# Performance work log

Hardware: AMD Instinct MI355X
Metric: run time of the kernel (lower is better)

The kernel has to match this reference:

```python
import jax, jax.numpy as jnp
import numpy as np

B, H = 1024, 1024
HID, RHID = 128, 64
DT = 1.0
EPS = 1e-6
SCALES = np.array([0.01, 0.02, 2000.0, 5.0], dtype=np.float32)  # R0[ohm], R1[ohm], C1[F], Q[Ah]


def analytic_ocv(soc):
    # smooth analytic open-circuit-voltage curve (Li-ion-like)
    return 3.0 + 1.2 * soc - 0.5 * soc * soc + 0.3 * soc * soc * soc


def setup_inputs() -> dict:
    key = jax.random.key(0)
    ks = jax.random.split(key, 12)
    inp = {
        "V": jax.random.normal(ks[0], (B, H), jnp.float32),
        "I": jax.random.normal(ks[1], (B, H), jnp.float32),
        "Tz": jax.random.normal(ks[2], (B, H), jnp.float32),
        "soc0": jax.random.uniform(ks[3], (B,), jnp.float32),
        # ParamHead: (soc, I, T) -> 4 positive ECM params
        "W1p": jax.random.normal(ks[4], (3, HID), jnp.float32) / np.sqrt(3.0),
        "b1p": jnp.zeros((HID,), jnp.float32),
        "W2p": jax.random.normal(ks[5], (HID, 4), jnp.float32) / np.sqrt(HID),
        "b2p": jnp.zeros((4,), jnp.float32),
        # ResidualNN: (soc, I, T) -> scalar voltage correction
        "W1r": jax.random.normal(ks[6], (3, RHID), jnp.float32) / np.sqrt(3.0),
        "b1r": jnp.zeros((RHID,), jnp.float32),
        "W2r": jax.random.normal(ks[7], (RHID, 1), jnp.float32) / np.sqrt(RHID),
        "b2r": jnp.zeros((1,), jnp.float32),
    }
    return inp


def _rollout(I, Tz, soc0, W1p, b1p, W2p, b2p, W1r, b1r, W2r, b2r):
    scales = jnp.asarray(SCALES)

    def step(carry, inp_t):
        soc, v1 = carry                       # (B,), (B,)
        I_t, T_t = inp_t                      # (B,), (B,)
        feats = jnp.stack([soc, I_t, T_t], axis=-1)  # (B,3)
        # ParamHead MLP -> positive params via softplus*scale + eps
        hp = jnp.tanh(feats @ W1p + b1p)
        params = jax.nn.softplus(hp @ W2p + b2p) * scales + EPS  # (B,4)
        R0, R1, C1, Q = params[:, 0], params[:, 1], params[:, 2], params[:, 3]
        # ResidualNN correction
        hr = jnp.tanh(feats @ W1r + b1r)
        resid = (hr @ W2r + b2r)[:, 0]        # (B,)
        # Euler ODE updates: RC polarization branch + coulomb counting
        v1_new = v1 + DT * (-v1 / (R1 * C1) + I_t / C1)
        soc_new = jnp.clip(soc - DT * I_t / (Q * 3600.0), 0.0, 1.0)
        V_pred = analytic_ocv(soc_new) - I_t * R0 - v1_new + resid
        return (soc_new, v1_new), V_pred

    carry0 = (soc0, jnp.zeros_like(soc0))
    xs = (I.T, Tz.T)                          # time-major (H,B)
    _, V_pred = jax.lax.scan(step, carry0, xs)
    return V_pred.T                           # (B,H)


def reference(V, I, Tz, soc0, W1p, b1p, W2p, b2p, W1r, b1r, W2r, b2r):
    soc0 = jnp.where(jnp.isnan(soc0), 0.8, soc0)  # default soc0=0.8 semantics
    return _rollout(I, Tz, soc0, W1p, b1p, W2p, b2p, W1r, b1r, W2r, b2r)
```

## Files before the change

kernel.cpp:

```cpp
#include <hip/hip_runtime.h>


#define NB 1024
#define HT 1024
#define HIDN 128
#define RHIDN 64

typedef unsigned uint2v __attribute__((ext_vector_type(2)));

__device__ __forceinline__ float readlane_f(float v, int lane) {
    int r = __builtin_amdgcn_readlane(__builtin_bit_cast(int, v), lane);
    return __builtin_bit_cast(float, r);
}

template <int CTRL, int RMASK>
__device__ __forceinline__ float dpp_add(float x) {
    int s = __builtin_amdgcn_update_dpp(0, __builtin_bit_cast(int, x),
                                        CTRL, RMASK, 0xF, true);
    return x + __builtin_bit_cast(float, s);
}

__device__ __forceinline__ void permlane32_swap(float& a, float& b) {
    uint2v r = __builtin_amdgcn_permlane32_swap(
        __builtin_bit_cast(unsigned, a), __builtin_bit_cast(unsigned, b),
        false, false);
    a = __builtin_bit_cast(float, r[0]);
    b = __builtin_bit_cast(float, r[1]);
}

__device__ __forceinline__ float swz_xor16(float x) {
    int r = __builtin_amdgcn_ds_swizzle(__builtin_bit_cast(int, x), 0x401F);
    return __builtin_bit_cast(float, r);
}

__device__ __forceinline__ float wave_sum(float x) {
    x = dpp_add<0x111, 0xF>(x);
    x = dpp_add<0x112, 0xF>(x);
    x = dpp_add<0x114, 0xF>(x);
    x = dpp_add<0x118, 0xF>(x);
    x = dpp_add<0x142, 0xA>(x);
    x = dpp_add<0x143, 0xC>(x);
    return readlane_f(x, 63);
}

__device__ __forceinline__ float tanh_fast(float x) {
    float t = __builtin_amdgcn_exp2f(x * 2.88539008177793f);
    float r = __builtin_amdgcn_rcpf(t + 1.0f);
    return fmaf(-2.0f, r, 1.0f);
}

__device__ __forceinline__ float softplus_fast(float x) {
    float e = __builtin_amdgcn_exp2f(x * 1.44269504088896f);
    return 0.693147180559945f * __builtin_amdgcn_logf(e + 1.0f);
}

__global__ __launch_bounds__(64, 1) void rollout_kernel(
    const float* __restrict__ Iin, const float* __restrict__ Tzin,
    const float* __restrict__ soc0,
    const float* __restrict__ W1p, const float* __restrict__ b1p,
    const float* __restrict__ W2p, const float* __restrict__ b2p,
    const float* __restrict__ W1r, const float* __restrict__ b1r,
    const float* __restrict__ W2r, const float* __restrict__ b2r,
    float* __restrict__ out)
{
    const int b    = blockIdx.x;
    const int lane = threadIdx.x;
    const int ja = lane, jb = lane + 64;
    const int row = lane >> 4;
    const bool oddrow = (row & 1) != 0;

    const float scaleLane = (row == 0) ? 0.01f : (row == 1) ? 2000.0f
                          : (row == 2) ? 0.02f : 5.0f;

    const float w1pa0 = W1p[0 * HIDN + ja], w1pa1 = W1p[1 * HIDN + ja], w1pa2 = W1p[2 * HIDN + ja];
    const float w1pb0 = W1p[0 * HIDN + jb], w1pb1 = W1p[1 * HIDN + jb], w1pb2 = W1p[2 * HIDN + jb];
    const float bpa = b1p[ja], bpb = b1p[jb];
    const float w2pa0 = W2p[ja * 4 + 0], w2pa1 = W2p[ja * 4 + 1],
                w2pa2 = W2p[ja * 4 + 2], w2pa3 = W2p[ja * 4 + 3];
    const float w2pb0 = W2p[jb * 4 + 0], w2pb1 = W2p[jb * 4 + 1],
                w2pb2 = W2p[jb * 4 + 2], w2pb3 = W2p[jb * 4 + 3];
    const float w1r0 = W1r[0 * RHIDN + lane], w1r1 = W1r[1 * RHIDN + lane], w1r2 = W1r[2 * RHIDN + lane];
    const float brr  = b1r[lane];
    const float w2rr = W2r[lane];
    const float b2p0 = b2p[0], b2p1 = b2p[1], b2p2 = b2p[2], b2p3 = b2p[3];
    const float b2rr = b2r[0];

    const float biasLane = (row == 0) ? b2p0 : (row == 1) ? b2p2
                         : (row == 2) ? b2p1 : b2p3;

    float socv = soc0[b];
    {   unsigned u = __builtin_bit_cast(unsigned, socv);
        if ((u & 0x7FFFFFFFu) > 0x7F800000u) socv = 0.8f; }
    float v1 = 0.0f;

    const float* Ib = Iin  + (size_t)b * HT;
    const float* Tb = Tzin + (size_t)b * HT;
    float*       Ob = out  + (size_t)b * HT;

    float Inext = Ib[lane];
    float Tnext = Tb[lane];

    for (int t0 = 0; t0 < HT; t0 += 64) {
        const float Ibuf = Inext;
        const float Tbuf = Tnext;
        const int t1 = t0 + 64;
        if (t1 < HT) { Inext = Ib[t1 + lane]; Tnext = Tb[t1 + lane]; }

        float Vbuf = 0.0f;
        #pragma unroll 4
        for (int s = 0; s < 64; ++s) {
            const float It = readlane_f(Ibuf, s);
            const float Tt = readlane_f(Tbuf, s);

            const float za = fmaf(Tt, w1pa2, fmaf(It, w1pa1, fmaf(socv, w1pa0, bpa)));
            const float zb = fmaf(Tt, w1pb2, fmaf(It, w1pb1, fmaf(socv, w1pb0, bpb)));
            const float ha = tanh_fast(za);
            const float hb = tanh_fast(zb);

            float p0 = fmaf(hb, w2pb0, ha * w2pa0);
            float p1 = fmaf(hb, w2pb1, ha * w2pa1);
            float p2 = fmaf(hb, w2pb2, ha * w2pa2);
            float p3 = fmaf(hb, w2pb3, ha * w2pa3);

            const float zr  = fmaf(Tt, w1r2, fmaf(It, w1r1, fmaf(socv, w1r0, brr)));
            const float prr = tanh_fast(zr) * w2rr;

            permlane32_swap(p0, p1); float ab = p0 + p1;
            permlane32_swap(p2, p3); float cd = p2 + p3;
            ab += swz_xor16(ab);
            cd += swz_xor16(cd);
            float z = oddrow ? cd : ab;
            z = dpp_add<0x111, 0xF>(z);
            z = dpp_add<0x112, 0xF>(z);
            z = dpp_add<0x114, 0xF>(z);
            z = dpp_add<0x118, 0xF>(z);

            const float resid = wave_sum(prr) + b2rr;

            const float sp   = softplus_fast(z + biasLane);
            const float par  = fmaf(sp, scaleLane, 1e-6f);
            const float ipar = __builtin_amdgcn_rcpf(par);
            const float R0    = readlane_f(par, 15);
            const float invC1 = readlane_f(ipar, 31);
            const float invR1 = readlane_f(ipar, 47);
            const float invQ  = readlane_f(ipar, 63);

            const float invR1C1 = invR1 * invC1;
            v1 = v1 + fmaf(-v1, invR1C1, It * invC1);

            socv = fmaf(It * invQ, -2.77777777777778e-4f, socv);
            socv = fminf(fmaxf(socv, 0.0f), 1.0f);

            const float ocv = fmaf(socv, fmaf(socv, fmaf(socv, 0.3f, -0.5f), 1.2f), 3.0f);
            const float Vp  = (fmaf(-It, R0, ocv) - v1) + resid;

            Vbuf = (lane == s) ? Vp : Vbuf;
        }
        Ob[t0 + lane] = Vbuf;
    }
}

extern "C" void kernel_launch(void* const* d_in, const int* in_sizes, int n_in,
                              void* d_out, int out_size, void* d_ws, size_t ws_size,
                              hipStream_t stream) {
    const float* Iin  = (const float*)d_in[1];
    const float* Tzin = (const float*)d_in[2];
    const float* soc0 = (const float*)d_in[3];
    const float* W1p  = (const float*)d_in[4];
    const float* b1p  = (const float*)d_in[5];
    const float* W2p  = (const float*)d_in[6];
    const float* b2p  = (const float*)d_in[7];
    const float* W1r  = (const float*)d_in[8];
    const float* b1r  = (const float*)d_in[9];
    const float* W2r  = (const float*)d_in[10];
    const float* b2r  = (const float*)d_in[11];
    float* out = (float*)d_out;

    hipLaunchKernelGGL(rollout_kernel, dim3(NB), dim3(64), 0, stream,
                       Iin, Tzin, soc0, W1p, b1p, W2p, b2p, W1r, b1r, W2r, b2r, out);
}
```

Before: 299.7 us.

## Offload residual MLP and output to second wave, pipelined over chunks

Measured after the change: 276.6 us. 1.08x faster.

```diff
diff --git a/kernel.cpp b/kernel.cpp
--- a/kernel.cpp
+++ b/kernel.cpp
@@ -4,7 +4,11 @@
 #define NB 1024
 #define HT 1024
 #define HIDN 128
-#define RHIDN 64
+#define NCHUNK 16
+
+#define K2  2.885390081777927f
+#define KL  1.4426950408889634f
+#define LN2 0.6931471805599453f
 
 typedef unsigned uint2v __attribute__((ext_vector_type(2)));
 
@@ -33,28 +37,13 @@
     return __builtin_bit_cast(float, r);
 }
 
-__device__ __forceinline__ float wave_sum(float x) {
-    x = dpp_add<0x111, 0xF>(x);
-    x = dpp_add<0x112, 0xF>(x);
-    x = dpp_add<0x114, 0xF>(x);
-    x = dpp_add<0x118, 0xF>(x);
-    x = dpp_add<0x142, 0xA>(x);
-    x = dpp_add<0x143, 0xC>(x);
-    return readlane_f(x, 63);
-}
-
-__device__ __forceinline__ float tanh_fast(float x) {
-    float t = __builtin_amdgcn_exp2f(x * 2.88539008177793f);
+__device__ __forceinline__ float tanh_ps(float z) {
+    float t = __builtin_amdgcn_exp2f(z);
     float r = __builtin_amdgcn_rcpf(t + 1.0f);
     return fmaf(-2.0f, r, 1.0f);
 }
 
-__device__ __forceinline__ float softplus_fast(float x) {
-    float e = __builtin_amdgcn_exp2f(x * 1.44269504088896f);
-    return 0.693147180559945f * __builtin_amdgcn_logf(e + 1.0f);
-}
-
-__global__ __launch_bounds__(64, 1) void rollout_kernel(
+__global__ __launch_bounds__(128, 1) void rollout_kernel(
     const float* __restrict__ Iin, const float* __restrict__ Tzin,
     const float* __restrict__ soc0,
     const float* __restrict__ W1p, const float* __restrict__ b1p,
@@ -64,99 +53,130 @@
     float* __restrict__ out)
 {
     const int b    = blockIdx.x;
-    const int lane = threadIdx.x;
-    const int ja = lane, jb = lane + 64;
-    const int row = lane >> 4;
-    const bool oddrow = (row & 1) != 0;
-
-    const float scaleLane = (row == 0) ? 0.01f : (row == 1) ? 2000.0f
-                          : (row == 2) ? 0.02f : 5.0f;
-
-    const float w1pa0 = W1p[0 * HIDN + ja], w1pa1 = W1p[1 * HIDN + ja], w1pa2 = W1p[2 * HIDN + ja];
-    const float w1pb0 = W1p[0 * HIDN + jb], w1pb1 = W1p[1 * HIDN + jb], w1pb2 = W1p[2 * HIDN + jb];
-    const float bpa = b1p[ja], bpb = b1p[jb];
-    const float w2pa0 = W2p[ja * 4 + 0], w2pa1 = W2p[ja * 4 + 1],
-                w2pa2 = W2p[ja * 4 + 2], w2pa3 = W2p[ja * 4 + 3];
-    const float w2pb0 = W2p[jb * 4 + 0], w2pb1 = W2p[jb * 4 + 1],
-                w2pb2 = W2p[jb * 4 + 2], w2pb3 = W2p[jb * 4 + 3];
-    const float w1r0 = W1r[0 * RHIDN + lane], w1r1 = W1r[1 * RHIDN + lane], w1r2 = W1r[2 * RHIDN + lane];
-    const float brr  = b1r[lane];
-    const float w2rr = W2r[lane];
-    const float b2p0 = b2p[0], b2p1 = b2p[1], b2p2 = b2p[2], b2p3 = b2p[3];
-    const float b2rr = b2r[0];
-
-    const float biasLane = (row == 0) ? b2p0 : (row == 1) ? b2p2
-                         : (row == 2) ? b2p1 : b2p3;
-
-    float socv = soc0[b];
-    {   unsigned u = __builtin_bit_cast(unsigned, socv);
-        if ((u & 0x7FFFFFFFu) > 0x7F800000u) socv = 0.8f; }
-    float v1 = 0.0f;
+    const int wid  = threadIdx.x >> 6;
+    const int lane = threadIdx.x & 63;
+
+    __shared__ float4 handBuf[2][64];
+    __shared__ float4 coefS[64];
+    __shared__ float  w2rS[64];
 
     const float* Ib = Iin  + (size_t)b * HT;
     const float* Tb = Tzin + (size_t)b * HT;
     float*       Ob = out  + (size_t)b * HT;
-
-    float Inext = Ib[lane];
-    float Tnext = Tb[lane];
-
-    for (int t0 = 0; t0 < HT; t0 += 64) {
-        const float Ibuf = Inext;
-        const float Tbuf = Tnext;
-        const int t1 = t0 + 64;
-        if (t1 < HT) { Inext = Ib[t1 + lane]; Tnext = Tb[t1 + lane]; }
-
-        float Vbuf = 0.0f;
-        #pragma unroll 4
-        for (int s = 0; s < 64; ++s) {
-            const float It = readlane_f(Ibuf, s);
-            const float Tt = readlane_f(Tbuf, s);
-
-            const float za = fmaf(Tt, w1pa2, fmaf(It, w1pa1, fmaf(socv, w1pa0, bpa)));
-            const float zb = fmaf(Tt, w1pb2, fmaf(It, w1pb1, fmaf(socv, w1pb0, bpb)));
-            const float ha = tanh_fast(za);
-            const float hb = tanh_fast(zb);
-
-            float p0 = fmaf(hb, w2pb0, ha * w2pa0);
-            float p1 = fmaf(hb, w2pb1, ha * w2pa1);
-            float p2 = fmaf(hb, w2pb2, ha * w2pa2);
-            float p3 = fmaf(hb, w2pb3, ha * w2pa3);
-
-            const float zr  = fmaf(Tt, w1r2, fmaf(It, w1r1, fmaf(socv, w1r0, brr)));
-            const float prr = tanh_fast(zr) * w2rr;
-
-            permlane32_swap(p0, p1); float ab = p0 + p1;
-            permlane32_swap(p2, p3); float cd = p2 + p3;
-            ab += swz_xor16(ab);
-            cd += swz_xor16(cd);
-            float z = oddrow ? cd : ab;
-            z = dpp_add<0x111, 0xF>(z);
-            z = dpp_add<0x112, 0xF>(z);
-            z = dpp_add<0x114, 0xF>(z);
-            z = dpp_add<0x118, 0xF>(z);
-
-            const float resid = wave_sum(prr) + b2rr;
-
-            const float sp   = softplus_fast(z + biasLane);
-            const float par  = fmaf(sp, scaleLane, 1e-6f);
-            const float ipar = __builtin_amdgcn_rcpf(par);
-            const float R0    = readlane_f(par, 15);
-            const float invC1 = readlane_f(ipar, 31);
-            const float invR1 = readlane_f(ipar, 47);
-            const float invQ  = readlane_f(ipar, 63);
-
-            const float invR1C1 = invR1 * invC1;
-            v1 = v1 + fmaf(-v1, invR1C1, It * invC1);
-
-            socv = fmaf(It * invQ, -2.77777777777778e-4f, socv);
-            socv = fminf(fmaxf(socv, 0.0f), 1.0f);
-
-            const float ocv = fmaf(socv, fmaf(socv, fmaf(socv, 0.3f, -0.5f), 1.2f), 3.0f);
-            const float Vp  = (fmaf(-It, R0, ocv) - v1) + resid;
-
-            Vbuf = (lane == s) ? Vp : Vbuf;
+    const float b2rr = b2r[0];
+
+    float w1pa0=0,w1pa1=0,w1pa2=0,bpa=0, w1pb0=0,w1pb1=0,w1pb2=0,bpb=0;
+    float w2pa0=0,w2pa1=0,w2pa2=0,w2pa3=0, w2pb0=0,w2pb1=0,w2pb2=0,w2pb3=0;
+    float biasLane=0, scaleLane=0;
+    float socv=0, v1=0, Inext=0, Tnext=0;
+    const int row = lane >> 4;
+    const bool oddrow = (row & 1) != 0;
+
+    if (wid == 0) {
+        const int ja = lane, jb = lane + 64;
+        w1pa0 = W1p[0*HIDN+ja]*K2; w1pa1 = W1p[1*HIDN+ja]*K2; w1pa2 = W1p[2*HIDN+ja]*K2;
+        w1pb0 = W1p[0*HIDN+jb]*K2; w1pb1 = W1p[1*HIDN+jb]*K2; w1pb2 = W1p[2*HIDN+jb]*K2;
+        bpa = b1p[ja]*K2; bpb = b1p[jb]*K2;
+        w2pa0 = W2p[ja*4+0]*KL; w2pa1 = W2p[ja*4+1]*KL;
+        w2pa2 = W2p[ja*4+2]*KL; w2pa3 = W2p[ja*4+3]*KL;
+        w2pb0 = W2p[jb*4+0]*KL; w2pb1 = W2p[jb*4+1]*KL;
+        w2pb2 = W2p[jb*4+2]*KL; w2pb3 = W2p[jb*4+3]*KL;
+        const float b2p0 = b2p[0], b2p1 = b2p[1], b2p2 = b2p[2], b2p3 = b2p[3];
+        biasLane  = ((row == 0) ? b2p0 : (row == 1) ? b2p2 : (row == 2) ? b2p1 : b2p3) * KL;
+        scaleLane = ((row == 0) ? 0.01f : (row == 1) ? 2000.0f : (row == 2) ? 0.02f : 5.0f) * LN2;
+
+        socv = soc0[b];
+        unsigned u = __builtin_bit_cast(unsigned, socv);
+        if ((u & 0x7FFFFFFFu) > 0x7F800000u) socv = 0.8f;
+        v1 = 0.0f;
+        Inext = Ib[lane];
+        Tnext = Tb[lane];
+    }
+
+    for (int c = 0; c <= NCHUNK; ++c) {
+        if (wid == 0) {
+            if (c < NCHUNK) {
+                const float Ibuf = Inext;
+                const float Tbuf = Tnext;
+                const int t1 = (c + 1) * 64;
+                if (t1 < HT) { Inext = Ib[t1 + lane]; Tnext = Tb[t1 + lane]; }
+
+                float4 hand = make_float4(0.f, 0.f, 0.f, 0.f);
+                #pragma unroll 4
+                for (int s = 0; s < 64; ++s) {
+                    const float It = readlane_f(Ibuf, s);
+                    const float Tt = readlane_f(Tbuf, s);
+                    const float carry = socv;
+
+                    const float za = fmaf(Tt, w1pa2, fmaf(It, w1pa1, fmaf(socv, w1pa0, bpa)));
+                    const float zb = fmaf(Tt, w1pb2, fmaf(It, w1pb1, fmaf(socv, w1pb0, bpb)));
+                    const float ha = tanh_ps(za);
+                    const float hb = tanh_ps(zb);
+
+                    float p0 = fmaf(hb, w2pb0, ha * w2pa0);
+                    float p1 = fmaf(hb, w2pb1, ha * w2pa1);
+                    float p2 = fmaf(hb, w2pb2, ha * w2pa2);
+                    float p3 = fmaf(hb, w2pb3, ha * w2pa3);
+
+                    permlane32_swap(p0, p1); float ab = p0 + p1;
+                    permlane32_swap(p2, p3); float cd = p2 + p3;
+                    ab += swz_xor16(ab);
+                    cd += swz_xor16(cd);
+                    float z = oddrow ? cd : ab;
+                    z = dpp_add<0x111, 0xF>(z);
+                    z = dpp_add<0x112, 0xF>(z);
+                    z = dpp_add<0x114, 0xF>(z);
+                    z = dpp_add<0x118, 0xF>(z);
+
+                    const float e   = __builtin_amdgcn_exp2f(z + biasLane);
+                    const float lg  = __builtin_amdgcn_logf(e + 1.0f);
+                    const float par = fmaf(lg, scaleLane, 1e-6f);
+                    const float ipar = __builtin_amdgcn_rcpf(par);
+                    const float R0    = readlane_f(par, 15);
+                    const float invC1 = readlane_f(ipar, 31);
+                    const float invR1 = readlane_f(ipar, 47);
+                    const float invQ  = readlane_f(ipar, 63);
+
+                    const float invR1C1 = invR1 * invC1;
+                    v1 = v1 + fmaf(-v1, invR1C1, It * invC1);
+                    socv = fmaf(It * invQ, -2.77777777777778e-4f, socv);
+                    socv = __builtin_amdgcn_fmed3f(socv, 0.0f, 1.0f);
+
+                    const bool m = (lane == s);
+                    hand.x = m ? carry : hand.x;
+                    hand.y = m ? socv  : hand.y;
+                    hand.z = m ? v1    : hand.z;
+                    hand.w = m ? R0    : hand.w;
+                }
+                handBuf[c & 1][lane] = hand;
+            }
+        } else {
+            if (c == 0) {
+                coefS[lane] = make_float4(W1r[0*64+lane]*K2, W1r[1*64+lane]*K2,
+                                          W1r[2*64+lane]*K2, b1r[lane]*K2);
+                w2rS[lane] = W2r[lane];
+            } else {
+                const int cc = c - 1;
+                const float4 h  = handBuf[cc & 1][lane];
+                const float  Is = Ib[cc * 64 + lane];
+                const float  Ts = Tb[cc * 64 + lane];
+
+                float acc = b2rr;
+                #pragma unroll 8
+                for (int j = 0; j < 64; ++j) {
+                    const float4 w  = coefS[j];
+                    const float  wr = w2rS[j];
+                    const float z  = fmaf(Ts, w.z, fmaf(Is, w.y, fmaf(h.x, w.x, w.w)));
+                    acc = fmaf(tanh_ps(z), wr, acc);
+                }
+
+                const float s1  = h.y;
+                const float ocv = fmaf(s1, fmaf(s1, fmaf(s1, 0.3f, -0.5f), 1.2f), 3.0f);
+                const float Vp  = (fmaf(-Is, h.w, ocv) - h.z) + acc;
+                Ob[cc * 64 + lane] = Vp;
+            }
         }
-        Ob[t0 + lane] = Vbuf;
+        __syncthreads();
     }
 }
 
@@ -176,6 +196,6 @@
     const float* b2r  = (const float*)d_in[11];
     float* out = (float*)d_out;
 
-    hipLaunchKernelGGL(rollout_kernel, dim3(NB), dim3(64), 0, stream,
+    hipLaunchKernelGGL(rollout_kernel, dim3(NB), dim3(128), 0, stream,
                        Iin, Tzin, soc0, W1p, b1p, W2p, b2p, W1r, b1r, W2r, b2r, out);
 }
```
